# Kernel optimization log

Hardware: AMD Instinct MI355X
Metric: run time of the kernel (lower is better)

Reference implementation:

```python
import jax, jax.numpy as jnp
import numpy as np

RBF_START = 0.0
RBF_END = 12.0
RBF_STEPS = 32
ENERGY_SCALE = 0.01


def setup_inputs() -> dict:
    key = jax.random.key(0)
    k1, k2, k3, k4 = jax.random.split(key, 4)
    B, L, R, E, F = 8, 128, 2048, RBF_STEPS, 64
    return {
        "lig_feat": jax.random.normal(k1, (B, L, E, F), dtype=jnp.float32),
        "rec_feat": jax.random.normal(k2, (B, R, E, F), dtype=jnp.float32),
        "lig_coord": jax.random.normal(k3, (B, L, 3), dtype=jnp.float32),
        "rec_coord": jax.random.normal(k4, (B, R, 3), dtype=jnp.float32),
    }


def reference(lig_feat, rec_feat, lig_coord, rec_coord):
    # atn_coefs: contract feature dim f -> [B, L, R, E]
    atn_coefs = jnp.einsum('blef,bref->blre', lig_feat, rec_feat)
    # pairwise distances [B, L, R]
    diff = lig_coord[:, :, None, :] - rec_coord[:, None, :, :]
    dists = jnp.sqrt(jnp.sum(diff * diff, axis=-1))
    # RBF expansion [B, L, R, E]
    mu = jnp.linspace(RBF_START, RBF_END, RBF_STEPS, dtype=jnp.float32)
    sigma = (RBF_START - RBF_END) / RBF_STEPS
    z = (dists[..., None] - mu) / sigma
    rbfs = jnp.exp(-(z * z))
    # per-entry scalar energy [B]
    U = jnp.sum(atn_coefs * rbfs * ENERGY_SCALE, axis=(1, 2, 3))
    return U
```

## Files before the change

### kernel.cpp

```cpp
#include <hip/hip_runtime.h>

#define NB 8
#define NL 128
#define NR 2048
#define NE 32
#define NF 64
#define RT 128
#define NRT (NR / RT)
#define EH 4
#define EPB (NE / EH)
#define NTHREADS 512
#define NWAVES (NTHREADS / 64)

typedef __attribute__((ext_vector_type(4)))  float f32x4;
typedef __attribute__((ext_vector_type(16))) float f32x16;
typedef __attribute__((ext_vector_type(8)))  short s16x8;
typedef __attribute__((ext_vector_type(2)))  unsigned int u32x2;

__device__ __forceinline__ unsigned bf16pair(float a, float b) {
    union { float f; unsigned u; } ua, ub; ua.f = a; ub.f = b;
    return __builtin_amdgcn_perm(ub.u + 0x8000u, ua.u + 0x8000u, 0x07060302u);
}

__device__ __forceinline__ u32x2 pack4(f32x4 v) {
    u32x2 r;
    r.x = bf16pair(v.x, v.y);
    r.y = bf16pair(v.z, v.w);
    return r;
}

__device__ __forceinline__ void async_load4(f32x4& r, const float* p) {
    asm volatile("global_load_dwordx4 %0, %1, off" : "=v"(r) : "v"(p) : "memory");
}

__global__ __launch_bounds__(NTHREADS, 2) void ff_kernel(
    const float* __restrict__ lig_feat,
    const float* __restrict__ rec_feat,
    const float* __restrict__ lig_coord,
    const float* __restrict__ rec_coord,
    float* __restrict__ out)
{
    __shared__ __align__(16) unsigned short sA[2][NL * NF];
    __shared__ __align__(16) unsigned short sB[2][RT * NF];
    __shared__ float sLc[3][NL];
    __shared__ float sRc[3][RT];
    __shared__ float sRed[NWAVES];

    const int blk = blockIdx.x;
    const int eh  = blk & (EH - 1);
    const int rt  = (blk >> 2) & (NRT - 1);
    const int b   = blk >> 6;
    const int e0  = eh * EPB;
    const int r0  = rt * RT;
    const int t   = threadIdx.x;
    const int lane = t & 63;
    const int wv   = t >> 6;

    const int f4    = t & 15;
    const int row00 = t >> 4;

    for (int i = t; i < 3 * NL; i += NTHREADS) {
        const int c = i >> 7, l = i & 127;
        sLc[c][l] = lig_coord[((long)b * NL + l) * 3 + c];
    }
    for (int i = t; i < 3 * RT; i += NTHREADS) {
        const int c = i >> 7, r = i & 127;
        sRc[c][r] = rec_coord[((long)b * NR + r0 + r) * 3 + c];
    }

    f32x4 tA[4], tB[4];
    #pragma unroll
    for (int j = 0; j < 4; ++j)
        tA[j] = *(const f32x4*)(lig_feat + (((long)b * NL + (row00 + 32 * j)) * NE + e0) * NF + f4 * 4);
    #pragma unroll
    for (int j = 0; j < 4; ++j)
        tB[j] = *(const f32x4*)(rec_feat + (((long)b * NR + r0 + (row00 + 32 * j)) * NE + e0) * NF + f4 * 4);

    __syncthreads();

    const int n  = lane & 31;
    const int h  = lane >> 5;
    const int tr  = wv & 3;
    const int tl0 = wv >> 2;
    const int colr = tr * 32 + n;
    const float rx = sRc[0][colr], ry = sRc[1][colr], rz = sRc[2][colr];
    float d[2][16];
    #pragma unroll
    for (int t2 = 0; t2 < 2; ++t2) {
        const int tl = tl0 + 2 * t2;
        #pragma unroll
        for (int i = 0; i < 16; ++i) {
            const int row = tl * 32 + 4 * h + (i & 3) + ((i >> 2) << 3);
            const float dx = sLc[0][row] - rx;
            const float dy = sLc[1][row] - ry;
            const float dz = sLc[2][row] - rz;
            d[t2][i] = sqrtf(dx * dx + dy * dy + dz * dz);
        }
    }

    #pragma unroll
    for (int j = 0; j < 4; ++j) {
        const int r = row00 + 32 * j;
        const int pos = (((f4 >> 1) ^ (r & 7)) << 3) + ((f4 & 1) << 2);
        *(u32x2*)&sA[0][r * NF + pos] = pack4(tA[j]);
    }
    #pragma unroll
    for (int j = 0; j < 4; ++j) {
        const int r = row00 + 32 * j;
        const int pos = (((f4 >> 1) ^ (r & 7)) << 3) + ((f4 & 1) << 2);
        *(u32x2*)&sB[0][r * NF + pos] = pack4(tB[j]);
    }
    if (EPB > 1) {
        #pragma unroll
        for (int j = 0; j < 4; ++j)
            async_load4(tA[j], lig_feat + (((long)b * NL + (row00 + 32 * j)) * NE + e0 + 1) * NF + f4 * 4);
        #pragma unroll
        for (int j = 0; j < 4; ++j)
            async_load4(tB[j], rec_feat + (((long)b * NR + r0 + (row00 + 32 * j)) * NE + e0 + 1) * NF + f4 * 4);
    }
    __syncthreads();

    const float inv_s = 32.0f / 12.0f;
    const int sw = n & 7;
    const int aRow = (tl0 * 32 + n) * NF;
    const int bRow = (tr * 32 + n) * NF;

    float sum = 0.0f;

    #pragma unroll
    for (int ep = 0; ep < EPB; ++ep) {
        const int cur = ep & 1;

        f32x16 acc0 = {0,0,0,0,0,0,0,0,0,0,0,0,0,0,0,0};
        f32x16 acc1 = acc0;
        #pragma unroll
        for (int kc = 0; kc < 4; ++kc) {
            const int off = (((kc * 2 + h) ^ sw) << 3);
            const s16x8 a0 = *(const s16x8*)&sA[cur][aRow + off];
            const s16x8 a1 = *(const s16x8*)&sA[cur][aRow + 64 * NF + off];
            const s16x8 bf = *(const s16x8*)&sB[cur][bRow + off];
            acc0 = __builtin_amdgcn_mfma_f32_32x32x16_bf16(a0, bf, acc0, 0, 0, 0);
            acc1 = __builtin_amdgcn_mfma_f32_32x32x16_bf16(a1, bf, acc1, 0, 0, 0);
        }
        const float nmu = -(float)(e0 + ep) * (32.0f / 31.0f);
        #pragma unroll
        for (int i = 0; i < 16; ++i) {
            float z;
            z = __builtin_fmaf(d[0][i], inv_s, nmu); sum += __expf(-z * z) * acc0[i];
            z = __builtin_fmaf(d[1][i], inv_s, nmu); sum += __expf(-z * z) * acc1[i];
        }

        if (ep + 1 < EPB) {
            asm volatile("s_waitcnt vmcnt(0)"
                         : "+v"(tA[0]), "+v"(tA[1]), "+v"(tA[2]), "+v"(tA[3]),
                           "+v"(tB[0]), "+v"(tB[1]), "+v"(tB[2]), "+v"(tB[3])
                         :: "memory");
            #pragma unroll
            for (int j = 0; j < 4; ++j) {
                const int r = row00 + 32 * j;
                const int pos = (((f4 >> 1) ^ (r & 7)) << 3) + ((f4 & 1) << 2);
                *(u32x2*)&sA[cur ^ 1][r * NF + pos] = pack4(tA[j]);
            }
            #pragma unroll
            for (int j = 0; j < 4; ++j) {
                const int r = row00 + 32 * j;
                const int pos = (((f4 >> 1) ^ (r & 7)) << 3) + ((f4 & 1) << 2);
                *(u32x2*)&sB[cur ^ 1][r * NF + pos] = pack4(tB[j]);
            }
            if (ep + 2 < EPB) {
                const int en = e0 + ep + 2;
                #pragma unroll
                for (int j = 0; j < 4; ++j)
                    async_load4(tA[j], lig_feat + (((long)b * NL + (row00 + 32 * j)) * NE + en) * NF + f4 * 4);
                #pragma unroll
                for (int j = 0; j < 4; ++j)
                    async_load4(tB[j], rec_feat + (((long)b * NR + r0 + (row00 + 32 * j)) * NE + en) * NF + f4 * 4);
            }
            __syncthreads();
        }
    }

    sum *= 0.01f;
    #pragma unroll
    for (int off = 32; off > 0; off >>= 1)
        sum += __shfl_down(sum, off, 64);
    if (lane == 0) sRed[wv] = sum;
    __syncthreads();
    if (t == 0) {
        float s = 0.f;
        #pragma unroll
        for (int w = 0; w < NWAVES; ++w) s += sRed[w];
        atomicAdd(&out[b], s);
    }
}

extern "C" void kernel_launch(void* const* d_in, const int* in_sizes, int n_in,
                              void* d_out, int out_size, void* d_ws, size_t ws_size,
                              hipStream_t stream) {
    const float* lig_feat  = (const float*)d_in[0];
    const float* rec_feat  = (const float*)d_in[1];
    const float* lig_coord = (const float*)d_in[2];
    const float* rec_coord = (const float*)d_in[3];
    float* out = (float*)d_out;

    hipMemsetAsync(out, 0, (size_t)out_size * sizeof(float), stream);

    dim3 grid(NB * NRT * EH);
    ff_kernel<<<grid, NTHREADS, 0, stream>>>(lig_feat, rec_feat,
                                             lig_coord, rec_coord, out);
}
```

Measured before the change: 206.5 us.

## Halve receptor tile to 64 rows with 256-thread blocks and pointer-stepped async loads

Shrinks the receptor tile from 128 to 64 rows and the block from 512 to 256 threads, which doubles the grid and raises the occupancy target to 3 blocks per CU. Each block still loads the full 128-row ligand tile, so ligand traffic per unit of receptor work doubles. The first-stage loads become asynchronous and overlap the distance computation, and load addresses are now precomputed pointers that advance by NF each step. The aim is more parallelism and better latency hiding, at the cost of extra ligand reads and a larger per-thread register footprint for load staging.

After: 283.7 us. +37.4%, slower.

```diff
diff --git a/kernel.cpp b/kernel.cpp
--- a/kernel.cpp
+++ b/kernel.cpp
@@ -5,12 +5,14 @@
 #define NR 2048
 #define NE 32
 #define NF 64
-#define RT 128
+#define RT 64
 #define NRT (NR / RT)
 #define EH 4
 #define EPB (NE / EH)
-#define NTHREADS 512
+#define NTHREADS 256
 #define NWAVES (NTHREADS / 64)
+#define AJ 8
+#define BJ 4
 
 typedef __attribute__((ext_vector_type(4)))  float f32x4;
 typedef __attribute__((ext_vector_type(16))) float f32x16;
@@ -33,7 +35,11 @@
     asm volatile("global_load_dwordx4 %0, %1, off" : "=v"(r) : "v"(p) : "memory");
 }
 
-__global__ __launch_bounds__(NTHREADS, 2) void ff_kernel(
+#define TIE "+v"(tA[0]), "+v"(tA[1]), "+v"(tA[2]), "+v"(tA[3]), \
+            "+v"(tA[4]), "+v"(tA[5]), "+v"(tA[6]), "+v"(tA[7]), \
+            "+v"(tB[0]), "+v"(tB[1]), "+v"(tB[2]), "+v"(tB[3])
+
+__global__ __launch_bounds__(NTHREADS, 3) void ff_kernel(
     const float* __restrict__ lig_feat,
     const float* __restrict__ rec_feat,
     const float* __restrict__ lig_coord,
@@ -49,7 +55,7 @@
     const int blk = blockIdx.x;
     const int eh  = blk & (EH - 1);
     const int rt  = (blk >> 2) & (NRT - 1);
-    const int b   = blk >> 6;
+    const int b   = blk >> 7;
     const int e0  = eh * EPB;
     const int r0  = rt * RT;
     const int t   = threadIdx.x;
@@ -64,24 +70,32 @@
         sLc[c][l] = lig_coord[((long)b * NL + l) * 3 + c];
     }
     for (int i = t; i < 3 * RT; i += NTHREADS) {
-        const int c = i >> 7, r = i & 127;
+        const int c = i >> 6, r = i & 63;
         sRc[c][r] = rec_coord[((long)b * NR + r0 + r) * 3 + c];
     }
 
-    f32x4 tA[4], tB[4];
-    #pragma unroll
-    for (int j = 0; j < 4; ++j)
-        tA[j] = *(const f32x4*)(lig_feat + (((long)b * NL + (row00 + 32 * j)) * NE + e0) * NF + f4 * 4);
-    #pragma unroll
-    for (int j = 0; j < 4; ++j)
-        tB[j] = *(const f32x4*)(rec_feat + (((long)b * NR + r0 + (row00 + 32 * j)) * NE + e0) * NF + f4 * 4);
+    const float* pa[AJ];
+    const float* pb[BJ];
+    #pragma unroll
+    for (int j = 0; j < AJ; ++j)
+        pa[j] = lig_feat + (((long)b * NL + (row00 + 16 * j)) * NE + e0) * NF + f4 * 4;
+    #pragma unroll
+    for (int j = 0; j < BJ; ++j)
+        pb[j] = rec_feat + (((long)b * NR + r0 + (row00 + 16 * j)) * NE + e0) * NF + f4 * 4;
+
+    f32x4 tA[AJ], tB[BJ];
+
+    #pragma unroll
+    for (int j = 0; j < AJ; ++j) { async_load4(tA[j], pa[j]); pa[j] += NF; }
+    #pragma unroll
+    for (int j = 0; j < BJ; ++j) { async_load4(tB[j], pb[j]); pb[j] += NF; }
 
     __syncthreads();
 
     const int n  = lane & 31;
     const int h  = lane >> 5;
-    const int tr  = wv & 3;
-    const int tl0 = wv >> 2;
+    const int tr  = wv & 1;
+    const int tl0 = wv >> 1;
     const int colr = tr * 32 + n;
     const float rx = sRc[0][colr], ry = sRc[1][colr], rz = sRc[2][colr];
     float d[2][16];
@@ -98,26 +112,24 @@
         }
     }
 
-    #pragma unroll
-    for (int j = 0; j < 4; ++j) {
-        const int r = row00 + 32 * j;
+    asm volatile("s_waitcnt vmcnt(0)" : TIE :: "memory");
+    #pragma unroll
+    for (int j = 0; j < AJ; ++j) {
+        const int r = row00 + 16 * j;
         const int pos = (((f4 >> 1) ^ (r & 7)) << 3) + ((f4 & 1) << 2);
         *(u32x2*)&sA[0][r * NF + pos] = pack4(tA[j]);
     }
     #pragma unroll
-    for (int j = 0; j < 4; ++j) {
-        const int r = row00 + 32 * j;
+    for (int j = 0; j < BJ; ++j) {
+        const int r = row00 + 16 * j;
         const int pos = (((f4 >> 1) ^ (r & 7)) << 3) + ((f4 & 1) << 2);
         *(u32x2*)&sB[0][r * NF + pos] = pack4(tB[j]);
     }
-    if (EPB > 1) {
-        #pragma unroll
-        for (int j = 0; j < 4; ++j)
-            async_load4(tA[j], lig_feat + (((long)b * NL + (row00 + 32 * j)) * NE + e0 + 1) * NF + f4 * 4);
-        #pragma unroll
-        for (int j = 0; j < 4; ++j)
-            async_load4(tB[j], rec_feat + (((long)b * NR + r0 + (row00 + 32 * j)) * NE + e0 + 1) * NF + f4 * 4);
-    }
+    #pragma unroll
+    for (int j = 0; j < AJ; ++j) { async_load4(tA[j], pa[j]); pa[j] += NF; }
+    #pragma unroll
+    for (int j = 0; j < BJ; ++j) { async_load4(tB[j], pb[j]); pb[j] += NF; }
+
     __syncthreads();
 
     const float inv_s = 32.0f / 12.0f;
@@ -130,6 +142,7 @@
     #pragma unroll
     for (int ep = 0; ep < EPB; ++ep) {
         const int cur = ep & 1;
+        const int nxt = cur ^ 1;
 
         f32x16 acc0 = {0,0,0,0,0,0,0,0,0,0,0,0,0,0,0,0};
         f32x16 acc1 = acc0;
@@ -151,30 +164,24 @@
         }
 
         if (ep + 1 < EPB) {
-            asm volatile("s_waitcnt vmcnt(0)"
-                         : "+v"(tA[0]), "+v"(tA[1]), "+v"(tA[2]), "+v"(tA[3]),
-                           "+v"(tB[0]), "+v"(tB[1]), "+v"(tB[2]), "+v"(tB[3])
-                         :: "memory");
+            asm volatile("s_waitcnt vmcnt(0)" : TIE :: "memory");
             #pragma unroll
-            for (int j = 0; j < 4; ++j) {
-                const int r = row00 + 32 * j;
+            for (int j = 0; j < AJ; ++j) {
+                const int r = row00 + 16 * j;
                 const int pos = (((f4 >> 1) ^ (r & 7)) << 3) + ((f4 & 1) << 2);
-                *(u32x2*)&sA[cur ^ 1][r * NF + pos] = pack4(tA[j]);
+                *(u32x2*)&sA[nxt][r * NF + pos] = pack4(tA[j]);
             }
             #pragma unroll
-            for (int j = 0; j < 4; ++j) {
-                const int r = row00 + 32 * j;
+            for (int j = 0; j < BJ; ++j) {
+                const int r = row00 + 16 * j;
                 const int pos = (((f4 >> 1) ^ (r & 7)) << 3) + ((f4 & 1) << 2);
-                *(u32x2*)&sB[cur ^ 1][r * NF + pos] = pack4(tB[j]);
+                *(u32x2*)&sB[nxt][r * NF + pos] = pack4(tB[j]);
             }
             if (ep + 2 < EPB) {
-                const int en = e0 + ep + 2;
                 #pragma unroll
-                for (int j = 0; j < 4; ++j)
-                    async_load4(tA[j], lig_feat + (((long)b * NL + (row00 + 32 * j)) * NE + en) * NF + f4 * 4);
+                for (int j = 0; j < AJ; ++j) { async_load4(tA[j], pa[j]); pa[j] += NF; }
                 #pragma unroll
-                for (int j = 0; j < 4; ++j)
-                    async_load4(tB[j], rec_feat + (((long)b * NR + r0 + (row00 + 32 * j)) * NE + en) * NF + f4 * 4);
+                for (int j = 0; j < BJ; ++j) { async_load4(tB[j], pb[j]); pb[j] += NF; }
             }
             __syncthreads();
         }
```
